# Kernel tuning notes

Measured on AMD Instinct MI355X. Metric: run time of the kernel, lower is better.

## Reference

```python
import jax, jax.numpy as jnp
import numpy as np

N_PAIR = 32
N_ENTI = 36          # VidVRD object classes (+pad)
N_CLS_TOT = 133      # 132 predicate classes + background id 0
NUM_BASE = 92        # split='base' -> pids 1..92
N_CTX = 8
MAX_L = 40           # GeneralAlproCfg.max_txt_len
D = 768


def setup_inputs() -> dict:
    key = jax.random.key(0)
    ks = jax.random.split(key, 11)
    std = 0.02
    return {
        "so_cls_ids": jax.random.randint(ks[0], (N_PAIR, 2), 0, N_ENTI, dtype=jnp.int64),
        "enti_txt_embds": jax.random.normal(ks[1], (N_ENTI, 256), jnp.float32),
        "prefix_embds": jax.random.normal(ks[2], (N_CLS_TOT, 1, D), jnp.float32) * std,
        "suffix_embds": jax.random.normal(ks[3], (N_CLS_TOT, MAX_L - 1 - N_CTX, D), jnp.float32) * std,
        "token_mask": jnp.ones((N_CLS_TOT, MAX_L), jnp.int32),
        "meta_ctx_embds": jax.random.normal(ks[4], (N_CTX, D), jnp.float32) * std,
        "subj_ctx_embds": jax.random.normal(ks[5], (N_CTX, D), jnp.float32) * std,
        "obj_ctx_embds": jax.random.normal(ks[6], (N_CTX, D), jnp.float32) * std,
        "W1": jax.random.normal(ks[7], (512, 256), jnp.float32) * std,
        "b1": jnp.zeros((256,), jnp.float32),
        "W2": jax.random.normal(ks[8], (256, 2 * D), jnp.float32) * std,
    }


def reference(so_cls_ids, enti_txt_embds, prefix_embds, suffix_embds, token_mask,
              meta_ctx_embds, subj_ctx_embds, obj_ctx_embds, W1, b1, W2):
    n_pair = so_cls_ids.shape[0]
    pids = jnp.arange(1, NUM_BASE + 1)                      # split='base'
    n_cls = NUM_BASE

    # entity text-embedding gather + tiny MLP
    s_embd = enti_txt_embds[so_cls_ids[:, 0]]               # [n_pair, 256]
    o_embd = enti_txt_embds[so_cls_ids[:, 1]]
    so = jnp.concatenate([s_embd, o_embd], axis=-1)         # [n_pair, 512]
    h = jax.nn.relu(so @ W1 + b1)                           # [n_pair, 256]
    so_e = h @ W2                                           # [n_pair, 1536]
    s_q, o_q = so_e[:, :D], so_e[:, D:]

    # softmax attention over meta context (keys = values = meta_ctx_embds)
    scale = 1.0 / jnp.sqrt(jnp.asarray(D, jnp.float32))
    s_att = jax.nn.softmax(s_q @ meta_ctx_embds.T * scale, axis=-1) @ meta_ctx_embds  # [n_pair, D]
    o_att = jax.nn.softmax(o_q @ meta_ctx_embds.T * scale, axis=-1) @ meta_ctx_embds

    s_ctx = subj_ctx_embds[None, :, :] + s_att[:, None, :]  # [n_pair, n_ctx, D]
    o_ctx = obj_ctx_embds[None, :, :] + o_att[:, None, :]

    prefix = prefix_embds[pids]                             # [n_cls, 1, D]
    suffix = suffix_embds[pids]                             # [n_cls, L_suf, D]
    l_suf = suffix.shape[1]

    def build(ctx):
        return jnp.concatenate([
            jnp.broadcast_to(prefix[None], (n_pair, n_cls, 1, D)),
            jnp.broadcast_to(ctx[:, None], (n_pair, n_cls, N_CTX, D)),
            jnp.broadcast_to(suffix[None], (n_pair, n_cls, l_suf, D)),
        ], axis=2).reshape(n_pair * n_cls, MAX_L, D)

    subj_token_embds = build(s_ctx)                         # [n_pair*n_cls, MAX_L, D]
    obj_token_embds = build(o_ctx)
    mask = jnp.tile(token_mask[pids], (n_pair, 1))          # [n_pair*n_cls, MAX_L]
    return subj_token_embds, obj_token_embds, mask
```

## Files before the change

kernel.cpp:

```cpp
#include <hip/hip_runtime.h>
#include <hip/hip_bf16.h>

typedef unsigned int u32;
typedef __attribute__((ext_vector_type(4))) float f32x4;

#define NPAIR 32
#define NCLS  92
#define NCTX  8
#define MAXL  40
#define DIM   768
#define LSUF  31

#define MAT_ELEMS 90439680u
#define MASK_BASE 180879360u

#define NBLK_CTX  256u
#define NBLK_D1   1472u
#define NBLK_MASK 115u
#define NBLK_ALL  (NBLK_CTX + NBLK_D1 + NBLK_MASK)

__global__ __launch_bounds__(256) void k_fused(
    const int* __restrict__ so_ids,
    const float* __restrict__ enti,
    const float* __restrict__ prefix,
    const float* __restrict__ suffix,
    const int* __restrict__ tok_mask,
    const float* __restrict__ meta,
    const float* __restrict__ sctx,
    const float* __restrict__ octx,
    const float* __restrict__ W1,
    const float* __restrict__ b1,
    const float* __restrict__ W2,
    float* __restrict__ out)
{
    const u32 bid = blockIdx.x;
    const u32 t = threadIdx.x;
    __shared__ __align__(16) float arena[8 * DIM];
    __shared__ int ids[2];

    if (bid < NBLK_CTX) {
        const u32 which = bid / 128u;
        const u32 rem = bid - which * 128u;
        const u32 pair = rem / 4u;
        const u32 cg = rem & 3u;

        if (t == 0) {
            bool is64 = true;
            for (int i = 1; i < 64; i += 2) is64 = is64 && (so_ids[i] == 0);
            if (is64) { ids[0] = so_ids[4 * pair]; ids[1] = so_ids[4 * pair + 2]; }
            else      { ids[0] = so_ids[2 * pair]; ids[1] = so_ids[2 * pair + 1]; }
        }
        __syncthreads();

        float* so_vec = arena;
        float* h      = arena + 512;
        float* red    = arena + 768;
        float* probs  = arena + 2816;

        so_vec[t]        = enti[ids[0] * 256 + t];
        so_vec[256 + t]  = enti[ids[1] * 256 + t];
        __syncthreads();

        {
            float acc = b1[t];
            const float* w = W1 + t;
            #pragma unroll 8
            for (int k = 0; k < 512; ++k)
                acc = fmaf(so_vec[k], w[(size_t)k * 256], acc);
            h[t] = fmaxf(acc, 0.f);
        }
        __syncthreads();

        float qr[3] = {0.f, 0.f, 0.f};
        {
            const float* w = W2 + which * DIM + t;
            #pragma unroll 4
            for (int k = 0; k < 256; ++k) {
                const float hk = h[k];
                #pragma unroll
                for (int i = 0; i < 3; ++i)
                    qr[i] = fmaf(hk, w[(size_t)k * 1536 + i * 256], qr[i]);
            }
        }

        #pragma unroll
        for (int c = 0; c < 8; ++c) {
            float pp = 0.f;
            #pragma unroll
            for (int i = 0; i < 3; ++i)
                pp = fmaf(qr[i], meta[c * DIM + t + 256 * i], pp);
            red[c * 256 + t] = pp;
        }
        __syncthreads();
        for (int s = 128; s > 0; s >>= 1) {
            if (t < (u32)s) {
                #pragma unroll
                for (int c = 0; c < 8; ++c)
                    red[c * 256 + t] += red[c * 256 + t + s];
            }
            __syncthreads();
        }
        if (t == 0) {
            const float scale = 0.036084391824351615f;
            float sc[8], m = -1e30f;
            #pragma unroll
            for (int c = 0; c < 8; ++c) { sc[c] = red[c * 256] * scale; m = fmaxf(m, sc[c]); }
            float sum = 0.f;
            #pragma unroll
            for (int c = 0; c < 8; ++c) { sc[c] = expf(sc[c] - m); sum += sc[c]; }
            const float inv = 1.f / sum;
            #pragma unroll
            for (int c = 0; c < 8; ++c) probs[c] = sc[c] * inv;
        }
        __syncthreads();

        float pr[8];
        #pragma unroll
        for (int c = 0; c < 8; ++c) pr[c] = probs[c];
        float att_d[3];
        #pragma unroll
        for (int i = 0; i < 3; ++i) {
            const int d = t + 256 * i;
            float a = 0.f;
            #pragma unroll
            for (int c = 0; c < 8; ++c)
                a = fmaf(pr[c], meta[c * DIM + d], a);
            att_d[i] = a;
        }
        __syncthreads();

        const float* ctxg = which ? octx : sctx;
        #pragma unroll
        for (int j = 0; j < 8; ++j) {
            #pragma unroll
            for (int i = 0; i < 3; ++i) {
                const int d = t + 256 * i;
                arena[j * DIM + d] = ctxg[j * DIM + d] + att_d[i];
            }
        }
        __syncthreads();

        float* base = out + (size_t)which * MAT_ELEMS
                          + ((size_t)(pair * NCLS) * MAXL + 1u) * DIM;
        for (u32 c = 0; c < 23u; ++c) {
            const u32 cls = cg * 23u + c;
            float* bc = base + (size_t)cls * (MAXL * DIM);
            #pragma unroll
            for (u32 uu = 0; uu < 6u; ++uu) {
                const u32 u = uu * 256u + t;
                __builtin_nontemporal_store(*(const f32x4*)(arena + u * 4u),
                                            (f32x4*)(bc + u * 4u));
            }
        }
    } else if (bid < NBLK_CTX + NBLK_D1) {
        const u32 r = bid - NBLK_CTX;
        const u32 which = r / (NCLS * 8u);
        const u32 rem = r - which * (NCLS * 8u);
        const u32 cls = rem / 8u;
        const u32 tq = rem - cls * 8u;

        for (u32 u = t; u < 4u * 192u; u += 256u) {
            const u32 j = u / 192u;
            const u32 dpos = u - j * 192u;
            const u32 rtok = (tq == 0u) ? (j == 0u ? 0u : 8u + j) : (8u + 4u * tq + j);
            const float* src = (rtok == 0u)
                ? (prefix + (size_t)(cls + 1u) * DIM + dpos * 4u)
                : (suffix + ((size_t)(cls + 1u) * LSUF + (rtok - 9u)) * DIM + dpos * 4u);
            *(f32x4*)(arena + u * 4u) = *(const f32x4*)src;
        }
        __syncthreads();

        for (u32 pair = 0; pair < NPAIR; ++pair) {
            float* slab = out + (size_t)which * MAT_ELEMS
                              + ((size_t)(pair * NCLS + cls) * MAXL) * DIM;
            #pragma unroll
            for (u32 uu = 0; uu < 3u; ++uu) {
                const u32 u = uu * 256u + t;
                const u32 j = u / 192u;
                const u32 dpos = u - j * 192u;
                const u32 rtok = (tq == 0u) ? (j == 0u ? 0u : 8u + j) : (8u + 4u * tq + j);
                __builtin_nontemporal_store(*(const f32x4*)(arena + u * 4u),
                    (f32x4*)(slab + (size_t)rtok * DIM + dpos * 4u));
            }
        }
    } else {
        const u32 idx4 = (bid - NBLK_CTX - NBLK_D1) * 256u + t;
        const u32 m = idx4 * 4u;
        f32x4 v;
        #pragma unroll
        for (int j = 0; j < 4; ++j) {
            const u32 i = m + (u32)j;
            const u32 rw = i / 40u;
            const u32 tk = i - rw * 40u;
            const u32 cls = rw % 92u;
            v[j] = (float)tok_mask[(cls + 1u) * 40u + tk];
        }
        __builtin_nontemporal_store(v, (f32x4*)(out + MASK_BASE + m));
    }
}

extern "C" void kernel_launch(void* const* d_in, const int* in_sizes, int n_in,
                              void* d_out, int out_size, void* d_ws, size_t ws_size,
                              hipStream_t stream) {
    const int* so_ids     = (const int*)d_in[0];
    const float* enti     = (const float*)d_in[1];
    const float* prefix   = (const float*)d_in[2];
    const float* suffix   = (const float*)d_in[3];
    const int* tok_mask   = (const int*)d_in[4];
    const float* meta     = (const float*)d_in[5];
    const float* sctx     = (const float*)d_in[6];
    const float* octx     = (const float*)d_in[7];
    const float* W1       = (const float*)d_in[8];
    const float* b1       = (const float*)d_in[9];
    const float* W2       = (const float*)d_in[10];

    k_fused<<<dim3(NBLK_ALL), dim3(256), 0, stream>>>(
        so_ids, enti, prefix, suffix, tok_mask, meta, sctx, octx, W1, b1, W2,
        (float*)d_out);
}
```

Measured before the change: 143.4 us.

## Split into context-prep kernel and linear grid-stride output sweep

The single fused kernel with heterogeneous block roles becomes two kernels. A small prep kernel computes the per-pair context sums into workspace. A grid-stride sweep kernel then writes the whole output in linear order with nontemporal float4 stores, gathering each element from prefix, sums or suffix by index decode. This aims for fully sequential, balanced write traffic, at the cost of an extra launch, a workspace round trip, and per-element integer division.

```diff
diff --git a/kernel.cpp b/kernel.cpp
--- a/kernel.cpp
+++ b/kernel.cpp
@@ -11,191 +11,161 @@
 #define DIM   768
 #define LSUF  31
 
-#define MAT_ELEMS 90439680u
-#define MASK_BASE 180879360u
+#define MAT_F4     22609920u
+#define MAT_F4_TOT 45219840u
+#define TOTAL_F4   45249280u
+#define GRID_SWEEP 2048u
+#define SWEEP_STRIDE (GRID_SWEEP * 256u)
 
-#define NBLK_CTX  256u
-#define NBLK_D1   1472u
-#define NBLK_MASK 115u
-#define NBLK_ALL  (NBLK_CTX + NBLK_D1 + NBLK_MASK)
-
-__global__ __launch_bounds__(256) void k_fused(
+__global__ __launch_bounds__(256) void k_prep(
     const int* __restrict__ so_ids,
     const float* __restrict__ enti,
-    const float* __restrict__ prefix,
-    const float* __restrict__ suffix,
-    const int* __restrict__ tok_mask,
     const float* __restrict__ meta,
     const float* __restrict__ sctx,
     const float* __restrict__ octx,
     const float* __restrict__ W1,
     const float* __restrict__ b1,
     const float* __restrict__ W2,
-    float* __restrict__ out)
+    float* __restrict__ sums)
 {
     const u32 bid = blockIdx.x;
     const u32 t = threadIdx.x;
-    __shared__ __align__(16) float arena[8 * DIM];
+    const u32 which = bid >> 5;
+    const u32 pair = bid & 31u;
+    __shared__ float arena[2824];
     __shared__ int ids[2];
 
-    if (bid < NBLK_CTX) {
-        const u32 which = bid / 128u;
-        const u32 rem = bid - which * 128u;
-        const u32 pair = rem / 4u;
-        const u32 cg = rem & 3u;
+    if (t == 0) {
+        bool is64 = true;
+        for (int i = 1; i < 64; i += 2) is64 = is64 && (so_ids[i] == 0);
+        if (is64) { ids[0] = so_ids[4 * pair]; ids[1] = so_ids[4 * pair + 2]; }
+        else      { ids[0] = so_ids[2 * pair]; ids[1] = so_ids[2 * pair + 1]; }
+    }
+    __syncthreads();
 
-        if (t == 0) {
-            bool is64 = true;
-            for (int i = 1; i < 64; i += 2) is64 = is64 && (so_ids[i] == 0);
-            if (is64) { ids[0] = so_ids[4 * pair]; ids[1] = so_ids[4 * pair + 2]; }
-            else      { ids[0] = so_ids[2 * pair]; ids[1] = so_ids[2 * pair + 1]; }
+    float* so_vec = arena;
+    float* h      = arena + 512;
+    float* red    = arena + 768;
+    float* probs  = arena + 2816;
+
+    so_vec[t]       = enti[ids[0] * 256 + t];
+    so_vec[256 + t] = enti[ids[1] * 256 + t];
+    __syncthreads();
+
+    {
+        float acc = b1[t];
+        const float* w = W1 + t;
+        #pragma unroll 8
+        for (int k = 0; k < 512; ++k)
+            acc = fmaf(so_vec[k], w[(size_t)k * 256], acc);
+        h[t] = fmaxf(acc, 0.f);
+    }
+    __syncthreads();
+
+    float qr[3] = {0.f, 0.f, 0.f};
+    {
+        const float* w = W2 + which * DIM + t;
+        #pragma unroll 4
+        for (int k = 0; k < 256; ++k) {
+            const float hk = h[k];
+            #pragma unroll
+            for (int i = 0; i < 3; ++i)
+                qr[i] = fmaf(hk, w[(size_t)k * 1536 + i * 256], qr[i]);
+        }
+    }
+
+    #pragma unroll
+    for (int c = 0; c < 8; ++c) {
+        float pp = 0.f;
+        #pragma unroll
+        for (int i = 0; i < 3; ++i)
+            pp = fmaf(qr[i], meta[c * DIM + t + 256 * i], pp);
+        red[c * 256 + t] = pp;
+    }
+    __syncthreads();
+    for (int s = 128; s > 0; s >>= 1) {
+        if (t < (u32)s) {
+            #pragma unroll
+            for (int c = 0; c < 8; ++c)
+                red[c * 256 + t] += red[c * 256 + t + s];
         }
         __syncthreads();
+    }
+    if (t == 0) {
+        const float scale = 0.036084391824351615f;
+        float sc[8], m = -1e30f;
+        #pragma unroll
+        for (int c = 0; c < 8; ++c) { sc[c] = red[c * 256] * scale; m = fmaxf(m, sc[c]); }
+        float sum = 0.f;
+        #pragma unroll
+        for (int c = 0; c < 8; ++c) { sc[c] = expf(sc[c] - m); sum += sc[c]; }
+        const float inv = 1.f / sum;
+        #pragma unroll
+        for (int c = 0; c < 8; ++c) probs[c] = sc[c] * inv;
+    }
+    __syncthreads();
 
-        float* so_vec = arena;
-        float* h      = arena + 512;
-        float* red    = arena + 768;
-        float* probs  = arena + 2816;
+    float pr[8];
+    #pragma unroll
+    for (int c = 0; c < 8; ++c) pr[c] = probs[c];
+    const float* ctxg = which ? octx : sctx;
+    float* dst = sums + (size_t)bid * (8u * DIM);
+    #pragma unroll
+    for (int i = 0; i < 3; ++i) {
+        const int d = t + 256 * i;
+        float a = 0.f;
+        #pragma unroll
+        for (int c = 0; c < 8; ++c)
+            a = fmaf(pr[c], meta[c * DIM + d], a);
+        #pragma unroll
+        for (int j = 0; j < 8; ++j)
+            dst[j * DIM + d] = ctxg[j * DIM + d] + a;
+    }
+}
 
-        so_vec[t]        = enti[ids[0] * 256 + t];
-        so_vec[256 + t]  = enti[ids[1] * 256 + t];
-        __syncthreads();
+__global__ __launch_bounds__(256) void k_sweep(
+    const float* __restrict__ prefix,
+    const float* __restrict__ suffix,
+    const int* __restrict__ tok_mask,
+    const float* __restrict__ sums,
+    float* __restrict__ out)
+{
+    const u32 tid0 = blockIdx.x * 256u + threadIdx.x;
+    const f32x4* pre4 = (const f32x4*)prefix;
+    const f32x4* suf4 = (const f32x4*)suffix;
+    const f32x4* sum4 = (const f32x4*)sums;
+    f32x4* out4 = (f32x4*)out;
 
-        {
-            float acc = b1[t];
-            const float* w = W1 + t;
-            #pragma unroll 8
-            for (int k = 0; k < 512; ++k)
-                acc = fmaf(so_vec[k], w[(size_t)k * 256], acc);
-            h[t] = fmaxf(acc, 0.f);
-        }
-        __syncthreads();
-
-        float qr[3] = {0.f, 0.f, 0.f};
-        {
-            const float* w = W2 + which * DIM + t;
-            #pragma unroll 4
-            for (int k = 0; k < 256; ++k) {
-                const float hk = h[k];
-                #pragma unroll
-                for (int i = 0; i < 3; ++i)
-                    qr[i] = fmaf(hk, w[(size_t)k * 1536 + i * 256], qr[i]);
+    for (u32 g = tid0; g < TOTAL_F4; g += SWEEP_STRIDE) {
+        f32x4 v;
+        if (g < MAT_F4_TOT) {
+            const u32 which = (g >= MAT_F4) ? 1u : 0u;
+            const u32 r = g - which * MAT_F4;
+            const u32 row = r / 192u;
+            const u32 dpos = r - row * 192u;
+            const u32 pair = row / 3680u;
+            const u32 rem = row - pair * 3680u;
+            const u32 cls = rem / 40u;
+            const u32 tok = rem - cls * 40u;
+            if (tok == 0u) {
+                v = pre4[(cls + 1u) * 192u + dpos];
+            } else if (tok < 9u) {
+                v = sum4[((which * NPAIR + pair) * 8u + (tok - 1u)) * 192u + dpos];
+            } else {
+                v = suf4[((cls + 1u) * LSUF + (tok - 9u)) * 192u + dpos];
+            }
+        } else {
+            const u32 m = (g - MAT_F4_TOT) * 4u;
+            #pragma unroll
+            for (int j = 0; j < 4; ++j) {
+                const u32 i = m + (u32)j;
+                const u32 rw = i / 40u;
+                const u32 tk = i - rw * 40u;
+                const u32 cls = rw % 92u;
+                v[j] = (float)tok_mask[(cls + 1u) * 40u + tk];
             }
         }
-
-        #pragma unroll
-        for (int c = 0; c < 8; ++c) {
-            float pp = 0.f;
-            #pragma unroll
-            for (int i = 0; i < 3; ++i)
-                pp = fmaf(qr[i], meta[c * DIM + t + 256 * i], pp);
-            red[c * 256 + t] = pp;
-        }
-        __syncthreads();
-        for (int s = 128; s > 0; s >>= 1) {
-            if (t < (u32)s) {
-                #pragma unroll
-                for (int c = 0; c < 8; ++c)
-                    red[c * 256 + t] += red[c * 256 + t + s];
-            }
-            __syncthreads();
-        }
-        if (t == 0) {
-            const float scale = 0.036084391824351615f;
-            float sc[8], m = -1e30f;
-            #pragma unroll
-            for (int c = 0; c < 8; ++c) { sc[c] = red[c * 256] * scale; m = fmaxf(m, sc[c]); }
-            float sum = 0.f;
-            #pragma unroll
-            for (int c = 0; c < 8; ++c) { sc[c] = expf(sc[c] - m); sum += sc[c]; }
-            const float inv = 1.f / sum;
-            #pragma unroll
-            for (int c = 0; c < 8; ++c) probs[c] = sc[c] * inv;
-        }
-        __syncthreads();
-
-        float pr[8];
-        #pragma unroll
-        for (int c = 0; c < 8; ++c) pr[c] = probs[c];
-        float att_d[3];
-        #pragma unroll
-        for (int i = 0; i < 3; ++i) {
-            const int d = t + 256 * i;
-            float a = 0.f;
-            #pragma unroll
-            for (int c = 0; c < 8; ++c)
-                a = fmaf(pr[c], meta[c * DIM + d], a);
-            att_d[i] = a;
-        }
-        __syncthreads();
-
-        const float* ctxg = which ? octx : sctx;
-        #pragma unroll
-        for (int j = 0; j < 8; ++j) {
-            #pragma unroll
-            for (int i = 0; i < 3; ++i) {
-                const int d = t + 256 * i;
-                arena[j * DIM + d] = ctxg[j * DIM + d] + att_d[i];
-            }
-        }
-        __syncthreads();
-
-        float* base = out + (size_t)which * MAT_ELEMS
-                          + ((size_t)(pair * NCLS) * MAXL + 1u) * DIM;
-        for (u32 c = 0; c < 23u; ++c) {
-            const u32 cls = cg * 23u + c;
-            float* bc = base + (size_t)cls * (MAXL * DIM);
-            #pragma unroll
-            for (u32 uu = 0; uu < 6u; ++uu) {
-                const u32 u = uu * 256u + t;
-                __builtin_nontemporal_store(*(const f32x4*)(arena + u * 4u),
-                                            (f32x4*)(bc + u * 4u));
-            }
-        }
-    } else if (bid < NBLK_CTX + NBLK_D1) {
-        const u32 r = bid - NBLK_CTX;
-        const u32 which = r / (NCLS * 8u);
-        const u32 rem = r - which * (NCLS * 8u);
-        const u32 cls = rem / 8u;
-        const u32 tq = rem - cls * 8u;
-
-        for (u32 u = t; u < 4u * 192u; u += 256u) {
-            const u32 j = u / 192u;
-            const u32 dpos = u - j * 192u;
-            const u32 rtok = (tq == 0u) ? (j == 0u ? 0u : 8u + j) : (8u + 4u * tq + j);
-            const float* src = (rtok == 0u)
-                ? (prefix + (size_t)(cls + 1u) * DIM + dpos * 4u)
-                : (suffix + ((size_t)(cls + 1u) * LSUF + (rtok - 9u)) * DIM + dpos * 4u);
-            *(f32x4*)(arena + u * 4u) = *(const f32x4*)src;
-        }
-        __syncthreads();
-
-        for (u32 pair = 0; pair < NPAIR; ++pair) {
-            float* slab = out + (size_t)which * MAT_ELEMS
-                              + ((size_t)(pair * NCLS + cls) * MAXL) * DIM;
-            #pragma unroll
-            for (u32 uu = 0; uu < 3u; ++uu) {
-                const u32 u = uu * 256u + t;
-                const u32 j = u / 192u;
-                const u32 dpos = u - j * 192u;
-                const u32 rtok = (tq == 0u) ? (j == 0u ? 0u : 8u + j) : (8u + 4u * tq + j);
-                __builtin_nontemporal_store(*(const f32x4*)(arena + u * 4u),
-                    (f32x4*)(slab + (size_t)rtok * DIM + dpos * 4u));
-            }
-        }
-    } else {
-        const u32 idx4 = (bid - NBLK_CTX - NBLK_D1) * 256u + t;
-        const u32 m = idx4 * 4u;
-        f32x4 v;
-        #pragma unroll
-        for (int j = 0; j < 4; ++j) {
-            const u32 i = m + (u32)j;
-            const u32 rw = i / 40u;
-            const u32 tk = i - rw * 40u;
-            const u32 cls = rw % 92u;
-            v[j] = (float)tok_mask[(cls + 1u) * 40u + tk];
-        }
-        __builtin_nontemporal_store(v, (f32x4*)(out + MASK_BASE + m));
+        __builtin_nontemporal_store(v, out4 + g);
     }
 }
 
@@ -213,8 +183,10 @@
     const float* W1       = (const float*)d_in[8];
     const float* b1       = (const float*)d_in[9];
     const float* W2       = (const float*)d_in[10];
+    float* sums = (float*)d_ws;
 
-    k_fused<<<dim3(NBLK_ALL), dim3(256), 0, stream>>>(
-        so_ids, enti, prefix, suffix, tok_mask, meta, sctx, octx, W1, b1, W2,
-        (float*)d_out);
+    k_prep<<<dim3(64), dim3(256), 0, stream>>>(
+        so_ids, enti, meta, sctx, octx, W1, b1, W2, sums);
+    k_sweep<<<dim3(GRID_SWEEP), dim3(256), 0, stream>>>(
+        prefix, suffix, tok_mask, sums, (float*)d_out);
 }
```

New measurement: 182.3 us. 27.2% more time.

## Split MLP/attention prep into separate kernel to avoid redundant per-block recompute

Applied to the files above, without the earlier changes.

The per-pair MLP, softmax attention and context sums were computed redundantly by 4 blocks per (which, pair) in the fused kernel. They now run once per (which, pair) in a 64-block prep kernel that writes the context rows to workspace, and the materialization kernel just loads them. This removes 4x redundant compute and the W1/W2 reads from the critical write blocks. The cost is an extra launch and a serialized dependency between the two kernels.

```diff
diff --git a/kernel.cpp b/kernel.cpp
--- a/kernel.cpp
+++ b/kernel.cpp
@@ -19,24 +19,122 @@
 #define NBLK_MASK 115u
 #define NBLK_ALL  (NBLK_CTX + NBLK_D1 + NBLK_MASK)
 
-__global__ __launch_bounds__(256) void k_fused(
+__global__ __launch_bounds__(256) void k_prep(
     const int* __restrict__ so_ids,
     const float* __restrict__ enti,
-    const float* __restrict__ prefix,
-    const float* __restrict__ suffix,
-    const int* __restrict__ tok_mask,
     const float* __restrict__ meta,
     const float* __restrict__ sctx,
     const float* __restrict__ octx,
     const float* __restrict__ W1,
     const float* __restrict__ b1,
     const float* __restrict__ W2,
+    float* __restrict__ sums)
+{
+    const u32 bid = blockIdx.x;
+    const u32 t = threadIdx.x;
+    const u32 which = bid >> 5;
+    const u32 pair = bid & 31u;
+    __shared__ float arena[2824];
+    __shared__ int ids[2];
+
+    if (t == 0) {
+        bool is64 = true;
+        for (int i = 1; i < 64; i += 2) is64 = is64 && (so_ids[i] == 0);
+        if (is64) { ids[0] = so_ids[4 * pair]; ids[1] = so_ids[4 * pair + 2]; }
+        else      { ids[0] = so_ids[2 * pair]; ids[1] = so_ids[2 * pair + 1]; }
+    }
+    __syncthreads();
+
+    float* so_vec = arena;
+    float* h      = arena + 512;
+    float* red    = arena + 768;
+    float* probs  = arena + 2816;
+
+    so_vec[t]       = enti[ids[0] * 256 + t];
+    so_vec[256 + t] = enti[ids[1] * 256 + t];
+    __syncthreads();
+
+    {
+        float acc = b1[t];
+        const float* w = W1 + t;
+        #pragma unroll 8
+        for (int k = 0; k < 512; ++k)
+            acc = fmaf(so_vec[k], w[(size_t)k * 256], acc);
+        h[t] = fmaxf(acc, 0.f);
+    }
+    __syncthreads();
+
+    float qr[3] = {0.f, 0.f, 0.f};
+    {
+        const float* w = W2 + which * DIM + t;
+        #pragma unroll 4
+        for (int k = 0; k < 256; ++k) {
+            const float hk = h[k];
+            #pragma unroll
+            for (int i = 0; i < 3; ++i)
+                qr[i] = fmaf(hk, w[(size_t)k * 1536 + i * 256], qr[i]);
+        }
+    }
+
+    #pragma unroll
+    for (int c = 0; c < 8; ++c) {
+        float pp = 0.f;
+        #pragma unroll
+        for (int i = 0; i < 3; ++i)
+            pp = fmaf(qr[i], meta[c * DIM + t + 256 * i], pp);
+        red[c * 256 + t] = pp;
+    }
+    __syncthreads();
+    for (int s = 128; s > 0; s >>= 1) {
+        if (t < (u32)s) {
+            #pragma unroll
+            for (int c = 0; c < 8; ++c)
+                red[c * 256 + t] += red[c * 256 + t + s];
+        }
+        __syncthreads();
+    }
+    if (t == 0) {
+        const float scale = 0.036084391824351615f;
+        float sc[8], m = -1e30f;
+        #pragma unroll
+        for (int c = 0; c < 8; ++c) { sc[c] = red[c * 256] * scale; m = fmaxf(m, sc[c]); }
+        float sum = 0.f;
+        #pragma unroll
+        for (int c = 0; c < 8; ++c) { sc[c] = expf(sc[c] - m); sum += sc[c]; }
+        const float inv = 1.f / sum;
+        #pragma unroll
+        for (int c = 0; c < 8; ++c) probs[c] = sc[c] * inv;
+    }
+    __syncthreads();
+
+    float pr[8];
+    #pragma unroll
+    for (int c = 0; c < 8; ++c) pr[c] = probs[c];
+    const float* ctxg = which ? octx : sctx;
+    float* dst = sums + (size_t)bid * (8u * DIM);
+    #pragma unroll
+    for (int i = 0; i < 3; ++i) {
+        const int d = t + 256 * i;
+        float a = 0.f;
+        #pragma unroll
+        for (int c = 0; c < 8; ++c)
+            a = fmaf(pr[c], meta[c * DIM + d], a);
+        #pragma unroll
+        for (int j = 0; j < 8; ++j)
+            dst[j * DIM + d] = ctxg[j * DIM + d] + a;
+    }
+}
+
+__global__ __launch_bounds__(256) void k_mat(
+    const float* __restrict__ prefix,
+    const float* __restrict__ suffix,
+    const int* __restrict__ tok_mask,
+    const float* __restrict__ sums,
     float* __restrict__ out)
 {
     const u32 bid = blockIdx.x;
     const u32 t = threadIdx.x;
     __shared__ __align__(16) float arena[8 * DIM];
-    __shared__ int ids[2];
 
     if (bid < NBLK_CTX) {
         const u32 which = bid / 128u;
@@ -44,100 +142,9 @@
         const u32 pair = rem / 4u;
         const u32 cg = rem & 3u;
 
-        if (t == 0) {
-            bool is64 = true;
-            for (int i = 1; i < 64; i += 2) is64 = is64 && (so_ids[i] == 0);
-            if (is64) { ids[0] = so_ids[4 * pair]; ids[1] = so_ids[4 * pair + 2]; }
-            else      { ids[0] = so_ids[2 * pair]; ids[1] = so_ids[2 * pair + 1]; }
-        }
-        __syncthreads();
-
-        float* so_vec = arena;
-        float* h      = arena + 512;
-        float* red    = arena + 768;
-        float* probs  = arena + 2816;
-
-        so_vec[t]        = enti[ids[0] * 256 + t];
-        so_vec[256 + t]  = enti[ids[1] * 256 + t];
-        __syncthreads();
-
-        {
-            float acc = b1[t];
-            const float* w = W1 + t;
-            #pragma unroll 8
-            for (int k = 0; k < 512; ++k)
-                acc = fmaf(so_vec[k], w[(size_t)k * 256], acc);
-            h[t] = fmaxf(acc, 0.f);
-        }
-        __syncthreads();
-
-        float qr[3] = {0.f, 0.f, 0.f};
-        {
-            const float* w = W2 + which * DIM + t;
-            #pragma unroll 4
-            for (int k = 0; k < 256; ++k) {
-                const float hk = h[k];
-                #pragma unroll
-                for (int i = 0; i < 3; ++i)
-                    qr[i] = fmaf(hk, w[(size_t)k * 1536 + i * 256], qr[i]);
-            }
-        }
-
-        #pragma unroll
-        for (int c = 0; c < 8; ++c) {
-            float pp = 0.f;
-            #pragma unroll
-            for (int i = 0; i < 3; ++i)
-                pp = fmaf(qr[i], meta[c * DIM + t + 256 * i], pp);
-            red[c * 256 + t] = pp;
-        }
-        __syncthreads();
-        for (int s = 128; s > 0; s >>= 1) {
-            if (t < (u32)s) {
-                #pragma unroll
-                for (int c = 0; c < 8; ++c)
-                    red[c * 256 + t] += red[c * 256 + t + s];
-            }
-            __syncthreads();
-        }
-        if (t == 0) {
-            const float scale = 0.036084391824351615f;
-            float sc[8], m = -1e30f;
-            #pragma unroll
-            for (int c = 0; c < 8; ++c) { sc[c] = red[c * 256] * scale; m = fmaxf(m, sc[c]); }
-            float sum = 0.f;
-            #pragma unroll
-            for (int c = 0; c < 8; ++c) { sc[c] = expf(sc[c] - m); sum += sc[c]; }
-            const float inv = 1.f / sum;
-            #pragma unroll
-            for (int c = 0; c < 8; ++c) probs[c] = sc[c] * inv;
-        }
-        __syncthreads();
-
-        float pr[8];
-        #pragma unroll
-        for (int c = 0; c < 8; ++c) pr[c] = probs[c];
-        float att_d[3];
-        #pragma unroll
-        for (int i = 0; i < 3; ++i) {
-            const int d = t + 256 * i;
-            float a = 0.f;
-            #pragma unroll
-            for (int c = 0; c < 8; ++c)
-                a = fmaf(pr[c], meta[c * DIM + d], a);
-            att_d[i] = a;
-        }
-        __syncthreads();
-
-        const float* ctxg = which ? octx : sctx;
-        #pragma unroll
-        for (int j = 0; j < 8; ++j) {
-            #pragma unroll
-            for (int i = 0; i < 3; ++i) {
-                const int d = t + 256 * i;
-                arena[j * DIM + d] = ctxg[j * DIM + d] + att_d[i];
-            }
-        }
+        const f32x4* src = (const f32x4*)(sums + (size_t)(which * NPAIR + pair) * (8u * DIM));
+        for (u32 u = t; u < 8u * 192u; u += 256u)
+            *(f32x4*)(arena + u * 4u) = src[u];
         __syncthreads();
 
         float* base = out + (size_t)which * MAT_ELEMS
@@ -213,8 +220,10 @@
     const float* W1       = (const float*)d_in[8];
     const float* b1       = (const float*)d_in[9];
     const float* W2       = (const float*)d_in[10];
-
-    k_fused<<<dim3(NBLK_ALL), dim3(256), 0, stream>>>(
-        so_ids, enti, prefix, suffix, tok_mask, meta, sctx, octx, W1, b1, W2,
-        (float*)d_out);
+    float* sums = (float*)d_ws;
+
+    k_prep<<<dim3(64), dim3(256), 0, stream>>>(
+        so_ids, enti, meta, sctx, octx, W1, b1, W2, sums);
+    k_mat<<<dim3(NBLK_ALL), dim3(256), 0, stream>>>(
+        prefix, suffix, tok_mask, sums, (float*)d_out);
 }
```

Result: slower. 187.0 us (+30.5%).
